# Kernel optimization log

Measured on AMD Instinct MI355X. Metric: run time of the kernel, lower is better.

Reference implementation:

```python
import jax, jax.numpy as jnp
import numpy as np

N = 48
E = N * (N - 1)
H_LSTM = 32
EPS = 20.0

def _conv1d(x, w, b):
    # x: [B, Cin, L], w: [Cout, Cin, K] -> [B, Cout, L], 'same' padding
    y = jax.lax.conv_general_dilated(x, w, window_strides=(1,), padding='SAME',
                                     dimension_numbers=('NCH', 'OIH', 'NCH'))
    return y + b[None, :, None]

def _map(M, x):
    # map_features: linear map along dim 0 (gather for n_to_e one-hot rows,
    # incidence-sum scatter for e_to_n). M: [O, I], x: [I, ...] -> [O, ...]
    return jnp.tensordot(M, x, axes=1)

def _node_cnn(x, adj, layers, final):
    # graph conv stack: neighbor mix (adj along dim 0) + conv1d over node axis + relu
    nl = len(layers)
    for i, (w, b) in enumerate(layers):
        x = _conv1d(_map(adj, x), w, b)
        if not (final and i == nl - 1):
            x = jax.nn.relu(x)
    return x

def _node_lstm(x, mem, adj, w, b):
    # mem = cat([c, h], dim=1); gates from conv over adj-mixed cat([x, h])
    H = mem.shape[1] // 2
    c, h = mem[:, :H], mem[:, H:]
    gates = _conv1d(_map(adj, jnp.concatenate([x, h], axis=1)), w, b)
    i, f, g, o = jnp.split(gates, 4, axis=1)
    c2 = jax.nn.sigmoid(f) * c + jax.nn.sigmoid(i) * jnp.tanh(g)
    h2 = jax.nn.sigmoid(o) * jnp.tanh(c2)
    return jnp.concatenate([c2, h2], axis=1)

def _forward(bi, bij, msgi, msgj, v, nmem0, emem0, neadj, eeadj,
             e_to_n0, e_to_n1, n_to_e0, n_to_e1, decoding, params):
    fm, efm, nlstm, elstm, pp, epp = params
    n = bi.shape[0]
    e = bij.shape[0]
    # map_node_feature_to_edge
    bi_g1 = _map(n_to_e0, bi)   # [E,1,N]
    bi_g2 = _map(n_to_e1, bi)   # [E,1,N]
    # softmax (logsumexp) message computation over bij [E,1,N,N]
    cmsgi = jax.nn.logsumexp((bi_g2[:, :, None, :] + bij) * EPS, axis=3) / EPS  # [E,1,N]
    cmsgj = jax.nn.logsumexp((bi_g1[:, :, :, None] + bij) * EPS, axis=2) / EPS  # [E,1,N]
    ncmsgi = _map(e_to_n0, cmsgi)
    ncmsgj = _map(e_to_n1, cmsgj)
    nnmsgi = _map(e_to_n0, msgi)
    nnmsgj = _map(e_to_n1, msgj)
    # partial_feature (detached in original)
    dec_mat = jax.nn.one_hot(decoding, n, dtype=bi.dtype)        # [N,N]
    xi = _map(n_to_e0, dec_mat)[:, :, None]                      # [E,N,1]
    xj = _map(n_to_e1, dec_mat)[:, None, :]                      # [E,1,N]
    ep = bij.reshape(e, n, n)
    f1 = jax.lax.stop_gradient(_map(e_to_n0, (ep * xi).sum(axis=1)).reshape(n, 1, n))
    f2 = jax.lax.stop_gradient(_map(e_to_n1, (ep * xj).sum(axis=2)).reshape(n, 1, n))
    node_feature = jnp.concatenate([bi, bi + v, nnmsgi, nnmsgj, ncmsgi, ncmsgj, f1, f2], axis=1)  # [N,8,N]
    edge_feature = jnp.concatenate([msgi, msgj, cmsgi, cmsgj, bi_g1, bi_g2], axis=1)              # [E,6,N]
    nfeat = _node_cnn(node_feature, neadj, fm, False)   # [N,32,N]
    efeat = _node_cnn(edge_feature, eeadj, efm, False)  # [E,32,N]
    ntoe1, ntoe2 = _map(n_to_e0, nfeat), _map(n_to_e1, nfeat)
    eton1, eton2 = _map(e_to_n0, efeat), _map(e_to_n1, efeat)
    nfeat = jnp.concatenate([nfeat, eton1, eton2], axis=1)  # [N,96,N]
    efeat = jnp.concatenate([efeat, ntoe1, ntoe2], axis=1)  # [E,96,N]
    nmem_new = _node_lstm(nfeat, nmem0, neadj, nlstm[0], nlstm[1])  # [N,64,N]
    emem_new = _node_lstm(efeat, emem0, eeadj, elstm[0], elstm[1])  # [E,64,N]
    nfeat = nmem_new[:, H_LSTM:]   # h part
    efeat = emem_new[:, H_LSTM:]
    ntoe1, ntoe2 = _map(n_to_e0, nfeat), _map(n_to_e1, nfeat)
    eton1, eton2 = _map(e_to_n0, efeat), _map(e_to_n1, efeat)
    nfeat = jnp.concatenate([nfeat, eton1, eton2], axis=1)
    efeat = jnp.concatenate([efeat, ntoe1, ntoe2], axis=1)
    efeat = _node_cnn(efeat, eeadj, epp, True)   # [E,2,N]
    nfeat = _node_cnn(nfeat, neadj, pp, True)    # [N,1,N]
    nmsgi = efeat[:, 0:1] + 0.5 * cmsgi - msgi
    nmsgj = efeat[:, 1:2] + 0.5 * cmsgj - msgj
    nv = nfeat.mean(axis=0, keepdims=True)       # [1,1,N]
    v_out = v + nv
    bij_out = bij - nmsgi.reshape(e, 1, n, 1) - nmsgj.reshape(e, 1, 1, n)
    bi_out = bi + _map(e_to_n0, nmsgi) + _map(e_to_n1, nmsgj) - nv
    msgi_out = msgi + nmsgi
    msgj_out = msgj + nmsgj
    # get_current_dual (softmax=True)
    cdual = (v_out.sum()
             + jax.nn.logsumexp(bi_out.reshape(-1, n) * EPS, axis=1).sum() / EPS
             + jax.nn.logsumexp(bij_out.reshape(-1, n * n) * EPS, axis=1).sum() / EPS)
    return bi_out, bij_out, msgi_out, msgj_out, v_out, cdual, nmem_new, emem_new, f1, f2

def setup_inputs() -> dict:
    key = jax.random.key(0)
    ks = jax.random.split(key, 16)
    ii, jj = np.meshgrid(np.arange(N), np.arange(N), indexing='ij')
    mask = ii != jj
    src, dst = ii[mask], jj[mask]  # [E] complete directed graph
    eye = np.eye(N, dtype=np.float32)
    n_to_e0 = jnp.asarray(eye[src])  # [E,N] one-hot gather
    n_to_e1 = jnp.asarray(eye[dst])
    e_to_n0 = n_to_e0.T              # [N,E] incidence scatter-sum
    e_to_n1 = n_to_e1.T
    def glorot(k, shape):
        fan_in = shape[1] * shape[2]
        return jax.random.normal(k, shape, jnp.float32) / np.sqrt(fan_in)
    pk = jax.random.split(ks[15], 20)
    return dict(
        bi=jax.random.normal(ks[0], (N, 1, N), jnp.float32),
        bij=jax.random.normal(ks[1], (E, 1, N, N), jnp.float32),
        msgi=jnp.zeros((E, 1, N), jnp.float32),
        msgj=jnp.zeros((E, 1, N), jnp.float32),
        v=jnp.zeros((1, 1, N), jnp.float32),
        nmem0=jnp.zeros((N, 2 * H_LSTM, N), jnp.float32),
        emem0=jnp.zeros((E, 2 * H_LSTM, N), jnp.float32),
        neadj=jax.random.uniform(ks[2], (N, N), jnp.float32) / N,
        eeadj=jax.random.uniform(ks[3], (E, E), jnp.float32) / E,
        e_to_n0=e_to_n0, e_to_n1=e_to_n1, n_to_e0=n_to_e0, n_to_e1=n_to_e1,
        decoding=jax.random.randint(ks[4], (N,), 0, N),
        fm_w0=glorot(pk[0], (32, 8, 3)), fm_b0=jnp.zeros((32,), jnp.float32),
        fm_w1=glorot(pk[1], (32, 32, 3)), fm_b1=jnp.zeros((32,), jnp.float32),
        efm_w0=glorot(pk[2], (32, 6, 3)), efm_b0=jnp.zeros((32,), jnp.float32),
        efm_w1=glorot(pk[3], (32, 32, 3)), efm_b1=jnp.zeros((32,), jnp.float32),
        nlstm_w=glorot(pk[4], (128, 128, 3)), nlstm_b=jnp.zeros((128,), jnp.float32),
        elstm_w=glorot(pk[5], (128, 128, 3)), elstm_b=jnp.zeros((128,), jnp.float32),
        pp_w0=glorot(pk[6], (16, 96, 3)), pp_b0=jnp.zeros((16,), jnp.float32),
        pp_w1=glorot(pk[7], (1, 16, 3)), pp_b1=jnp.zeros((1,), jnp.float32),
        epp_w0=glorot(pk[8], (16, 96, 3)), epp_b0=jnp.zeros((16,), jnp.float32),
        epp_w1=glorot(pk[9], (2, 16, 3)), epp_b1=jnp.zeros((2,), jnp.float32),
    )

def reference(bi, bij, msgi, msgj, v, nmem0, emem0, neadj, eeadj,
              e_to_n0, e_to_n1, n_to_e0, n_to_e1, decoding,
              fm_w0, fm_b0, fm_w1, fm_b1, efm_w0, efm_b0, efm_w1, efm_b1,
              nlstm_w, nlstm_b, elstm_w, elstm_b,
              pp_w0, pp_b0, pp_w1, pp_b1, epp_w0, epp_b0, epp_w1, epp_b1):
    params = ([(fm_w0, fm_b0), (fm_w1, fm_b1)],
              [(efm_w0, efm_b0), (efm_w1, efm_b1)],
              (nlstm_w, nlstm_b), (elstm_w, elstm_b),
              [(pp_w0, pp_b0), (pp_w1, pp_b1)],
              [(epp_w0, epp_b0), (epp_w1, epp_b1)])
    return _forward(bi, bij, msgi, msgj, v, nmem0, emem0, neadj, eeadj,
                    e_to_n0, e_to_n1, n_to_e0, n_to_e1, decoding, params)
```

## Files before the change

### kernel.cpp

```cpp
#include <hip/hip_runtime.h>
#include <cstdint>
#include <cstddef>

#define EE 2256
#define EP 2304

typedef __attribute__((ext_vector_type(8))) short bf16x8;
typedef __attribute__((ext_vector_type(4))) float f32x4;

__device__ __forceinline__ unsigned short f2b(float f){
  unsigned u = __builtin_bit_cast(unsigned, f);
  u += 0x7fffu + ((u>>16)&1u);
  return (unsigned short)(u>>16);
}
__device__ __forceinline__ float b2f(unsigned short h){
  unsigned u = ((unsigned)h)<<16; return __builtin_bit_cast(float, u);
}
__device__ __forceinline__ float sigm(float x){ return 1.f/(1.f+__expf(-x)); }
__device__ __forceinline__ float tanhfast(float x){ return 1.f - 2.f/(__expf(2.f*x)+1.f); }

__device__ __forceinline__ int xcd_swz(int bid, int nwg){
  int xcd = bid & 7, idx = bid >> 3;
  int q = nwg >> 3, r = nwg & 7;
  return (xcd < r ? xcd*(q+1) : r*(q+1) + (xcd-r)*q) + idx;
}

typedef __attribute__((address_space(3))) unsigned int lds_u32;
typedef __attribute__((address_space(1))) const unsigned int gbl_u32;
__device__ __forceinline__ void glds16(const void* g, void* l){
  __builtin_amdgcn_global_load_lds((gbl_u32*)g, (lds_u32*)l, 16, 0, 0);
}

__global__ __launch_bounds__(128) void gm_zero_pads(unsigned short* yp6, unsigned short* yp32,
                                                    unsigned short* yp16){
  int e = blockIdx.x; int tid = threadIdx.x;
  #pragma unroll
  for (int r=0; r<2; ++r){
    int row = r ? 49 : 0;
    if (tid < 8)  yp6 [((size_t)e*50+row)*8  + tid] = 0;
    if (tid < 32) yp32[((size_t)e*50+row)*32 + tid] = 0;
    if (tid < 16) yp16[((size_t)e*50+row)*16 + tid] = 0;
  }
}

__global__ __launch_bounds__(128) void gm_zero_pad128(unsigned short* yp128){
  int e = blockIdx.x; int tid = threadIdx.x;
  yp128[((size_t)e*50+0)*128 + tid] = 0;
  yp128[((size_t)e*50+49)*128 + tid] = 0;
}

__global__ void gm_prep_eeadj(const float* __restrict__ src, unsigned short* __restrict__ dst){
  int idx = blockIdx.x*256 + threadIdx.x;
  if (idx >= EP*EP) return;
  int r = idx / EP, k = idx - r*EP;
  float v = (r < EE && k < EE) ? src[(size_t)r*EE + k] : 0.f;
  dst[idx] = f2b(v);
}

__global__ void gm_prep_wall(const float* __restrict__ w0, const float* __restrict__ w1,
                             const float* __restrict__ w2, const float* __restrict__ w3,
                             const float* __restrict__ w4,
                             unsigned short* d0, unsigned short* d1, unsigned short* d2,
                             unsigned short* d3, unsigned short* d4){
  int idx = blockIdx.x*256 + threadIdx.x;
  const float* w; unsigned short* dp; int Co,Cin,KPT,Kpad,loc;
  if      (idx < 1024) { w=w0; dp=d0; Co=32;  Cin=6;   KPT=8;   Kpad=32;  loc=idx; }
  else if (idx < 4096) { w=w1; dp=d1; Co=32;  Cin=32;  KPT=32;  Kpad=96;  loc=idx-1024; }
  else if (idx < 53248){ w=w2; dp=d2; Co=128; Cin=128; KPT=128; Kpad=384; loc=idx-4096; }
  else if (idx < 57856){ w=w3; dp=d3; Co=16;  Cin=96;  KPT=96;  Kpad=288; loc=idx-53248; }
  else if (idx < 58880){ w=w4; dp=d4; Co=2;   Cin=16;  KPT=16;  Kpad=64;  loc=idx-57856; }
  else return;
  int co = loc / Kpad; int k = loc - co*Kpad;
  int t = k / KPT; int ci = k - t*KPT;
  float v = (co < Co && t < 3 && ci < Cin) ? w[((size_t)co*Cin + ci)*3 + t] : 0.f;
  dp[loc] = f2b(v);
}

__global__ __launch_bounds__(128) void gm_cmsg(const float* __restrict__ bi, const float* __restrict__ bij,
                                               float* __restrict__ cmi, float* __restrict__ cmj){
  int e = blockIdx.x; int tid = threadIdx.x;
  __shared__ float t[48*49]; __shared__ float bs[48], bd[48];
  const float* src = bij + (size_t)e*2304;
  for (int i=tid;i<2304;i+=128){ int r=i/48, c=i-r*48; t[r*49+c]=src[i]; }
  if (tid<48){ int s=e/47, m=e-s*47; int d=m+(m>=s); bs[tid]=bi[s*48+tid]; bd[tid]=bi[d*48+tid]; }
  __syncthreads();
  if (tid < 48){
    float mx=-1e30f;
    for (int n=0;n<48;n++) mx = fmaxf(mx, t[tid*49+n]+bd[n]);
    float sm=0.f;
    for (int n=0;n<48;n++) sm += __expf((t[tid*49+n]+bd[n]-mx)*20.f);
    cmi[e*48+tid] = mx + __logf(sm)*(1.f/20.f);
  } else if (tid>=64 && tid<112){
    int n = tid-64;
    float mx=-1e30f;
    for (int k=0;k<48;k++) mx = fmaxf(mx, t[k*49+n]+bs[k]);
    float sm=0.f;
    for (int k=0;k<48;k++) sm += __expf((t[k*49+n]+bs[k]-mx)*20.f);
    cmj[e*48+n] = mx + __logf(sm)*(1.f/20.f);
  }
}

__global__ __launch_bounds__(256) void gm_node_accum(const float* __restrict__ bij, const float* __restrict__ cmi,
                              const float* __restrict__ cmj, const float* __restrict__ msgi,
                              const float* __restrict__ msgj, const int* __restrict__ dec,
                              float* ncmi, float* ncmj, float* nnmi, float* nnmj,
                              float* o_f1, float* o_f2){
  int i = blockIdx.x; int tid = threadIdx.x;
  __shared__ float red[5][6][48];
  int mg = tid / 48;
  int w  = tid - mg*48;
  if (mg < 5){
    int dc = dec[i];
    float a1=0,a2=0,a3=0,a4=0,s1=0,s2=0;
    for (int m=mg; m<47; m+=5){
      int e1 = i*47+m;
      a1 += cmi[e1*48+w]; a3 += msgi[e1*48+w];
      s1 += bij[(size_t)e1*2304 + dc*48 + w];
      int j = m + (m>=i); int e2 = j*47 + i - (i>j);
      a2 += cmj[e2*48+w]; a4 += msgj[e2*48+w];
      s2 += bij[(size_t)e2*2304 + w*48 + dc];
    }
    red[mg][0][w]=a1; red[mg][1][w]=a2; red[mg][2][w]=a3;
    red[mg][3][w]=a4; red[mg][4][w]=s1; red[mg][5][w]=s2;
  }
  __syncthreads();
  if (tid < 48){
    float a1=0,a2=0,a3=0,a4=0,s1=0,s2=0;
    for (int g=0; g<5; g++){
      a1+=red[g][0][tid]; a2+=red[g][1][tid]; a3+=red[g][2][tid];
      a4+=red[g][3][tid]; s1+=red[g][4][tid]; s2+=red[g][5][tid];
    }
    ncmi[i*48+tid]=a1; ncmj[i*48+tid]=a2; nnmi[i*48+tid]=a3; nnmj[i*48+tid]=a4;
    o_f1[i*48+tid]=s1; o_f2[i*48+tid]=s2;
  }
}

__global__ void gm_build_x6(const float* __restrict__ msgi, const float* __restrict__ msgj,
                            const float* __restrict__ cmi, const float* __restrict__ cmj,
                            const float* __restrict__ bi, unsigned short* __restrict__ x6){
  int idx = blockIdx.x*256 + threadIdx.x;
  if (idx >= 288*EP) return;
  int row = idx / EP, e = idx - row*EP;
  int w = row / 6, c = row - w*6;
  unsigned short val = 0;
  if (e < EE){
    int s = e/47, m = e-s*47, d = m + (m>=s);
    float x;
    switch(c){
      case 0: x = msgi[e*48+w]; break;
      case 1: x = msgj[e*48+w]; break;
      case 2: x = cmi[e*48+w]; break;
      case 3: x = cmj[e*48+w]; break;
      case 4: x = bi[s*48+w]; break;
      default: x = bi[d*48+w]; break;
    }
    val = f2b(x);
  }
  x6[idx] = val;
}

__global__ void gm_fill_x128_hi(const float* __restrict__ emem0, const float* __restrict__ nfeat,
                                unsigned short* __restrict__ x128){
  int idx = blockIdx.x*256 + threadIdx.x;
  if (idx >= 96*EP) return;
  int q = idx/EP; int c = 32 + q; int e = idx - q*EP;
  if (e >= EE){ for (int w=0;w<48;w++) x128[(size_t)(w*128+c)*EP + e] = 0; return; }
  int s=e/47, m=e-s*47, d=m+(m>=s);
  const float* srcrow;
  if (c < 64)      srcrow = nfeat + ((size_t)s*32 + (c-32))*48;
  else if (c < 96) srcrow = nfeat + ((size_t)d*32 + (c-64))*48;
  else             srcrow = emem0 + ((size_t)e*64 + (c-64))*48;
  #pragma unroll
  for (int w4=0; w4<12; w4++){
    float4 xv = *(const float4*)(srcrow + w4*4);
    x128[(size_t)((w4*4+0)*128+c)*EP + e] = f2b(xv.x);
    x128[(size_t)((w4*4+1)*128+c)*EP + e] = f2b(xv.y);
    x128[(size_t)((w4*4+2)*128+c)*EP + e] = f2b(xv.z);
    x128[(size_t)((w4*4+3)*128+c)*EP + e] = f2b(xv.w);
  }
}

__global__ __launch_bounds__(256) void gm_map_gemm(
    const unsigned short* __restrict__ A, const unsigned short* __restrict__ BT,
    unsigned short* __restrict__ ypad, float* __restrict__ outf,
    const float* __restrict__ bias, int nrow, int Nvalid, int Cch, int Cslab,
    int do_relu, int f32_out)
{
  __shared__ __align__(16) unsigned short lA[128*32];
  __shared__ __align__(16) unsigned short lB[128*32];
  const int tid = threadIdx.x;
  const int lane = tid & 63, wid = tid >> 6;
  const int swz = xcd_swz(blockIdx.x, gridDim.x);
  const int m0 = (swz % nrow) * 128;
  const int n0 = (swz / nrow) * 128;
  const int wm = wid >> 1, wn = wid & 1;
  f32x4 acc[4][4];
  #pragma unroll
  for (int i=0;i<4;i++){
    #pragma unroll
    for (int j=0;j<4;j++) acc[i][j] = f32x4{0.f,0.f,0.f,0.f};
  }
  const int srow = (lane>>2), scol = (lane&3);

  for (int ks = 0; ks < EP/32; ++ks) {
    #pragma unroll
    for (int q=0;q<2;q++){
      int chunk = wid*2+q;
      int row = chunk*16 + srow;
      int off = (scol*16) ^ (((row>>1)&3)<<4);
      glds16((const char*)A  + (size_t)(m0+row)*(EP*2) + ks*64 + off, (char*)lA + chunk*1024);
      glds16((const char*)BT + (size_t)(n0+row)*(EP*2) + ks*64 + off, (char*)lB + chunk*1024);
    }
    __syncthreads();
    bf16x8 af[4], bfr[4];
    #pragma unroll
    for (int mi=0;mi<4;mi++){
      int row = wm*64 + mi*16 + (lane&15);
      int off = ((lane>>4)*16) ^ (((row>>1)&3)<<4);
      af[mi] = *(const bf16x8*)((const char*)lA + row*64 + off);
    }
    #pragma unroll
    for (int ni=0;ni<4;ni++){
      int row = wn*64 + ni*16 + (lane&15);
      int off = ((lane>>4)*16) ^ (((row>>1)&3)<<4);
      bfr[ni] = *(const bf16x8*)((const char*)lB + row*64 + off);
    }
    #pragma unroll
    for (int mi=0;mi<4;mi++){
      #pragma unroll
      for (int ni=0;ni<4;ni++)
        acc[mi][ni] = __builtin_amdgcn_mfma_f32_16x16x32_bf16(af[mi], bfr[ni], acc[mi][ni], 0,0,0);
    }
    __syncthreads();
  }
  #pragma unroll
  for (int mi=0;mi<4;mi++){
    int ebase = m0 + wm*64 + mi*16 + (lane>>4)*4;
    #pragma unroll
    for (int ni=0;ni<4;ni++){
      int c = n0 + wn*64 + ni*16 + (lane&15);
      if (c >= Nvalid) continue;
      int w = c / Cch, ci = c - w*Cch;
      float bv = bias ? bias[ci] : 0.f;
      #pragma unroll
      for (int r=0;r<4;r++){
        int e = ebase + r;
        if (e >= EE) continue;
        float x = acc[mi][ni][r] + bv;
        if (do_relu) x = fmaxf(x, 0.f);
        if (f32_out) outf[(size_t)e*Nvalid + c] = x;
        else ypad[((size_t)e*50 + 1 + w)*Cslab + ci] = f2b(x);
      }
    }
  }
}

__global__ __launch_bounds__(256) void gm_map_sk(
    const unsigned short* __restrict__ A, const unsigned short* __restrict__ BT,
    float* __restrict__ pbuf, int nrow, int ncol, int S, int kspan)
{
  __shared__ __align__(16) unsigned short lA[128*32];
  __shared__ __align__(16) unsigned short lB[128*32];
  const int tid = threadIdx.x;
  const int lane = tid & 63, wid = tid >> 6;
  const int swz = xcd_swz(blockIdx.x, gridDim.x);
  const int ntile = nrow*ncol;
  const int sp = swz / ntile;
  const int tile = swz - sp*ntile;
  const int m0 = (tile % nrow) * 128;
  const int n0 = (tile / nrow) * 128;
  const int Npad = ncol*128;
  const int k0 = sp*kspan, k1 = k0 + kspan;
  const int wm = wid >> 1, wn = wid & 1;
  f32x4 acc[4][4];
  #pragma unroll
  for (int i=0;i<4;i++){
    #pragma unroll
    for (int j=0;j<4;j++) acc[i][j] = f32x4{0.f,0.f,0.f,0.f};
  }
  const int srow = (lane>>2), scol = (lane&3);

  for (int ks = k0; ks < k1; ++ks){
    #pragma unroll
    for (int q=0;q<2;q++){
      int chunk = wid*2+q;
      int row = chunk*16 + srow;
      int off = (scol*16) ^ (((row>>1)&3)<<4);
      glds16((const char*)A  + (size_t)(m0+row)*(EP*2) + ks*64 + off, (char*)lA + chunk*1024);
      glds16((const char*)BT + (size_t)(n0+row)*(EP*2) + ks*64 + off, (char*)lB + chunk*1024);
    }
    __syncthreads();
    bf16x8 af[4], bfr[4];
    #pragma unroll
    for (int mi=0;mi<4;mi++){
      int row = wm*64 + mi*16 + (lane&15);
      int off = ((lane>>4)*16) ^ (((row>>1)&3)<<4);
      af[mi] = *(const bf16x8*)((const char*)lA + row*64 + off);
    }
    #pragma unroll
    for (int ni=0;ni<4;ni++){
      int row = wn*64 + ni*16 + (lane&15);
      int off = ((lane>>4)*16) ^ (((row>>1)&3)<<4);
      bfr[ni] = *(const bf16x8*)((const char*)lB + row*64 + off);
    }
    #pragma unroll
    for (int mi=0;mi<4;mi++){
      #pragma unroll
      for (int ni=0;ni<4;ni++)
        acc[mi][ni] = __builtin_amdgcn_mfma_f32_16x16x32_bf16(af[mi], bfr[ni], acc[mi][ni], 0,0,0);
    }
    __syncthreads();
  }
  float* pb = pbuf + (size_t)sp*2304*Npad;
  #pragma unroll
  for (int mi=0;mi<4;mi++){
    int ebase = m0 + wm*64 + mi*16 + (lane>>4)*4;
    #pragma unroll
    for (int ni=0;ni<4;ni++){
      int c = n0 + wn*64 + ni*16 + (lane&15);
      #pragma unroll
      for (int r=0;r<4;r++)
        pb[(size_t)(ebase+r)*Npad + c] = acc[mi][ni][r];
    }
  }
}

__global__ void gm_sk_fin(const float* __restrict__ pbuf, unsigned short* __restrict__ ypad,
                          float* __restrict__ outf, const float* __restrict__ bias,
                          int S, int Npad, int Nvalid, int Cch, int Cslab, int do_relu, int f32_out){
  int idx = blockIdx.x*256 + threadIdx.x;
  if (idx >= EE*Nvalid) return;
  int e = idx / Nvalid, c = idx - e*Nvalid;
  float s = 0.f;
  for (int p=0;p<S;p++) s += pbuf[(size_t)p*2304*Npad + (size_t)e*Npad + c];
  int w = c / Cch, ci = c - w*Cch;
  if (bias) s += bias[ci];
  if (do_relu) s = fmaxf(s, 0.f);
  if (f32_out) outf[(size_t)e*Nvalid + c] = s;
  else ypad[((size_t)e*50 + 1 + w)*Cslab + ci] = f2b(s);
}

template<int BM>
__global__ __launch_bounds__(256) void gm_conv_gemm(
    const unsigned short* __restrict__ Wp, const unsigned short* __restrict__ ypad,
    unsigned short* __restrict__ outT, const float* __restrict__ bias,
    int Cch, int KPT, int Kpad, int Co, int Ct, int do_relu)
{
  constexpr int MI = (BM==128)?4:((BM==32)?2:1);
  constexpr int NI = (BM==128)?4:2;
  __shared__ __align__(16) unsigned short lA[BM*32];
  __shared__ __align__(16) unsigned short lB[128*32];
  const int tid = threadIdx.x, lane = tid&63, wid = tid>>6;
  const int swz = xcd_swz(blockIdx.x, 864);
  const int e0 = (swz / 48) * 128;
  const int w  = swz % 48;
  const int rowb = (BM==128)? (wid>>1)*64 : 0;
  const int colb = (BM==128)? (wid&1)*64 : wid*32;
  f32x4 acc[MI][NI];
  #pragma unroll
  for (int i=0;i<MI;i++){
    #pragma unroll
    for (int j=0;j<NI;j++) acc[i][j] = f32x4{0.f,0.f,0.f,0.f};
  }
  const int srow=(lane>>2), scol=(lane&3);
  const int ksteps = Kpad/32;
  for (int ks=0; ks<ksteps; ++ks){
    for (int c = wid; c < BM/16; c += 4){
      int row = c*16 + srow;
      int off = (scol*16) ^ (((row>>1)&3)<<4);
      glds16((const char*)Wp + (size_t)row*(Kpad*2) + ks*64 + off, (char*)lA + c*1024);
    }
    for (int c = wid; c < 8; c += 4){
      int row = c*16 + srow;
      int off = (scol*16) ^ (((row>>1)&3)<<4);
      int kg = ks*32 + (off>>1);
      int t = kg / KPT;
      int ci = kg - t*KPT;
      int e = e0 + row;
      const char* src;
      if (t < 3 && e < EE) src = (const char*)ypad + ((size_t)(e*50 + w + t)*Cch + ci)*2;
      else                 src = (const char*)ypad;
      glds16(src, (char*)lB + c*1024);
    }
    __syncthreads();
    bf16x8 af[MI], bfr[NI];
    #pragma unroll
    for (int mi=0;mi<MI;mi++){
      int row = rowb + mi*16 + (lane&15);
      int off = ((lane>>4)*16) ^ (((row>>1)&3)<<4);
      af[mi] = *(const bf16x8*)((const char*)lA + row*64 + off);
    }
    #pragma unroll
    for (int ni=0;ni<NI;ni++){
      int row = colb + ni*16 + (lane&15);
      int off = ((lane>>4)*16) ^ (((row>>1)&3)<<4);
      bfr[ni] = *(const bf16x8*)((const char*)lB + row*64 + off);
    }
    #pragma unroll
    for (int mi=0;mi<MI;mi++){
      #pragma unroll
      for (int ni=0;ni<NI;ni++)
        acc[mi][ni] = __builtin_amdgcn_mfma_f32_16x16x32_bf16(af[mi], bfr[ni], acc[mi][ni], 0,0,0);
    }
    __syncthreads();
  }
  #pragma unroll
  for (int mi=0;mi<MI;mi++){
    #pragma unroll
    for (int ni=0;ni<NI;ni++){
      int m = colb + ni*16 + (lane&15);
      int e = e0 + m;
      if (e >= EE) continue;
      #pragma unroll
      for (int r=0;r<4;r++){
        int co = rowb + mi*16 + (lane>>4)*4 + r;
        if (co >= Co) continue;
        float x = acc[mi][ni][r] + (bias ? bias[co] : 0.f);
        if (do_relu) x = fmaxf(x, 0.f);
        outT[((size_t)(w*Ct + co))*EP + e] = f2b(x);
      }
    }
  }
}

__global__ void gm_build_nf(const float* __restrict__ bi, const float* __restrict__ v,
                            const float* __restrict__ nnmi, const float* __restrict__ nnmj,
                            const float* __restrict__ ncmi, const float* __restrict__ ncmj,
                            const float* __restrict__ f1, const float* __restrict__ f2,
                            float* __restrict__ nf){
  int idx = blockIdx.x*256+threadIdx.x;
  if (idx >= 48*8*48) return;
  int i = idx/(8*48); int rem = idx - i*(8*48); int c = rem/48; int w = rem-c*48;
  int iw = i*48+w;
  float x;
  switch(c){
    case 0: x=bi[iw]; break;
    case 1: x=bi[iw]+v[w]; break;
    case 2: x=nnmi[iw]; break;
    case 3: x=nnmj[iw]; break;
    case 4: x=ncmi[iw]; break;
    case 5: x=ncmj[iw]; break;
    case 6: x=f1[iw]; break;
    default: x=f2[iw]; break;
  }
  nf[idx]=x;
}

__global__ void gm_nmap(const float* __restrict__ adj, const float* __restrict__ X,
                        float* __restrict__ Y, int C){
  int idx = blockIdx.x*256 + threadIdx.x;
  int tot = 48*C*48;
  if (idx >= tot) return;
  int i = idx/(C*48); int rem = idx - i*(C*48);
  float s=0.f;
  for (int j=0;j<48;j++) s += adj[i*48+j]*X[(size_t)j*C*48 + rem];
  Y[idx]=s;
}

__global__ void gm_nconv(const float* __restrict__ X, const float* __restrict__ wgt,
                         const float* __restrict__ bias, float* __restrict__ Y,
                         int Cin, int Co, int relu){
  int idx = blockIdx.x*256 + threadIdx.x;
  int tot = 48*Co*48;
  if (idx >= tot) return;
  int i = idx/(Co*48); int rem = idx - i*(Co*48); int co = rem/48; int w = rem-co*48;
  float s = bias[co];
  const float* xb = X + (size_t)i*Cin*48;
  const float* wb = wgt + (size_t)co*Cin*3;
  for (int ci=0; ci<Cin; ++ci){
    float w0 = wb[ci*3], w1 = wb[ci*3+1], w2 = wb[ci*3+2];
    const float* xr = xb + ci*48;
    if (w > 0) s += xr[w-1]*w0;
    s += xr[w]*w1;
    if (w < 47) s += xr[w+1]*w2;
  }
  if (relu) s = fmaxf(s, 0.f);
  Y[idx] = s;
}

__global__ __launch_bounds__(256) void gm_nconv_lstm(const float* __restrict__ X,
    const float* __restrict__ wgt, const float* __restrict__ bias,
    const float* __restrict__ nmem0, float* __restrict__ o_nmem, float* __restrict__ nfeat2){
  int idx = blockIdx.x*256 + threadIdx.x;
  if (idx >= 48*32*48) return;
  int i = idx/(32*48); int rem = idx - i*(32*48); int ch = rem/48; int w = rem-ch*48;
  const float* xb = X + (size_t)i*128*48;
  float s0=bias[ch], s1=bias[32+ch], s2=bias[64+ch], s3=bias[96+ch];
  for (int ci=0; ci<128; ++ci){
    const float* xr = xb + ci*48;
    float xm = (w>0)? xr[w-1] : 0.f;
    float xc = xr[w];
    float xp = (w<47)? xr[w+1] : 0.f;
    const float* wb0 = wgt + ((size_t)ch*128+ci)*3;
    const float* wb1 = wgt + ((size_t)(32+ch)*128+ci)*3;
    const float* wb2 = wgt + ((size_t)(64+ch)*128+ci)*3;
    const float* wb3 = wgt + ((size_t)(96+ch)*128+ci)*3;
    s0 += xm*wb0[0]+xc*wb0[1]+xp*wb0[2];
    s1 += xm*wb1[0]+xc*wb1[1]+xp*wb1[2];
    s2 += xm*wb2[0]+xc*wb2[1]+xp*wb2[2];
    s3 += xm*wb3[0]+xc*wb3[1]+xp*wb3[2];
  }
  float c = nmem0[((size_t)i*64+ch)*48+w];
  float c2 = sigm(s1)*c + sigm(s0)*tanhfast(s2);
  float h2 = sigm(s3)*tanhfast(c2);
  o_nmem[((size_t)i*64+ch)*48+w] = c2;
  o_nmem[((size_t)i*64+32+ch)*48+w] = h2;
  nfeat2[((size_t)i*32+ch)*48+w] = h2;
}

__global__ __launch_bounds__(256) void gm_eton_x128(const unsigned short* __restrict__ x128,
                                                    float* __restrict__ xn){
  int row = blockIdx.x;
  int w = row >> 5, cc = row & 31;
  __shared__ float L[2256];
  const unsigned short* src = x128 + (size_t)(w*128 + cc)*EP;
  for (int t=threadIdx.x; t<2256; t+=256) L[t] = b2f(src[t]);
  __syncthreads();
  int tid = threadIdx.x;
  if (tid < 48){
    int i = tid; float s=0.f;
    for (int m=0;m<47;m++) s += L[i*47+m];
    xn[((size_t)i*128 + 32 + cc)*48 + w] = s;
  } else if (tid >= 64 && tid < 112){
    int i = tid-64; float s=0.f;
    for (int m=0;m<47;m++){
      int j = m + (m>=i);
      s += L[j*47 + i - (i>j)];
    }
    xn[((size_t)i*128 + 64 + cc)*48 + w] = s;
  }
}

__global__ void gm_xnode_copy(const float* __restrict__ nfeat, const float* __restrict__ nmem0,
                              float* __restrict__ xn){
  int idx = blockIdx.x*256+threadIdx.x;
  if (idx >= 48*64*48) return;
  int i = idx/(64*48); int rem = idx - i*(64*48); int c = rem/48; int w = rem-c*48;
  if (c < 32) xn[((size_t)i*128 + c)*48 + w] = nfeat[((size_t)i*32+c)*48+w];
  else        xn[((size_t)i*128 + 96 + (c-32))*48 + w] = nmem0[((size_t)i*64 + 32 + (c-32))*48 + w];
}

__global__ __launch_bounds__(256) void gm_elstm_pw(const unsigned short* __restrict__ gatesT,
                                                   const float* __restrict__ emem0,
                                                   float* __restrict__ o_emem){
  int bid = blockIdx.x;
  int e4 = bid / 6, chunk = bid - e4*6;
  int cw = chunk*256 + threadIdx.x;
  int ch = cw / 48, w = cw - ch*48;
  int ebase = e4*4;
  const unsigned short* g0 = gatesT + (size_t)(w*128 + ch)*EP + ebase;
  ushort4 vi = *(const ushort4*)(g0);
  ushort4 vf = *(const ushort4*)(g0 + (size_t)32*EP);
  ushort4 vg = *(const ushort4*)(g0 + (size_t)64*EP);
  ushort4 vo = *(const ushort4*)(g0 + (size_t)96*EP);
  const unsigned short* pi = (const unsigned short*)&vi;
  const unsigned short* pf = (const unsigned short*)&vf;
  const unsigned short* pg = (const unsigned short*)&vg;
  const unsigned short* po = (const unsigned short*)&vo;
  #pragma unroll
  for (int r=0;r<4;r++){
    int e = ebase + r;
    float gi = b2f(pi[r]), gf = b2f(pf[r]), gg = b2f(pg[r]), go = b2f(po[r]);
    float c  = emem0[((size_t)e*64 + ch)*48 + w];
    float c2 = sigm(gf)*c + sigm(gi)*tanhfast(gg);
    float h2 = sigm(go)*tanhfast(c2);
    o_emem[((size_t)e*64 + ch)*48 + w] = c2;
    o_emem[((size_t)e*64 + 32+ch)*48 + w] = h2;
  }
}

__global__ __launch_bounds__(256) void gm_eton_h(const float* __restrict__ o_emem,
                                                 float* __restrict__ x2){
  int row = blockIdx.x; int w = row >> 5, cc = row & 31;
  __shared__ float L[2256];
  for (int t=threadIdx.x; t<2256; t+=256)
    L[t] = o_emem[((size_t)t*64 + 32 + cc)*48 + w];
  __syncthreads();
  int tid = threadIdx.x;
  if (tid < 48){
    int i=tid; float s=0.f;
    for (int m=0;m<47;m++) s += L[i*47+m];
    x2[((size_t)i*96 + 32 + cc)*48 + w] = s;
  } else if (tid>=64 && tid<112){
    int i=tid-64; float s=0.f;
    for (int m=0;m<47;m++){ int j=m+(m>=i); s += L[j*47 + i - (i>j)]; }
    x2[((size_t)i*96 + 64 + cc)*48 + w] = s;
  }
}

__global__ void gm_x2_copy(const float* __restrict__ nfeat2, float* __restrict__ x2){
  int idx = blockIdx.x*256+threadIdx.x;
  if (idx >= 48*32*48) return;
  int i = idx/(32*48); int rem = idx - i*(32*48); int c = rem/48; int w = rem-c*48;
  x2[((size_t)i*96 + c)*48 + w] = nfeat2[idx];
}

__global__ __launch_bounds__(128) void gm_build_xpp(const float* __restrict__ o_emem,
                                                    const float* __restrict__ nfeat2,
                                                    unsigned short* __restrict__ xpp){
  int e = blockIdx.x; int tid = threadIdx.x;
  __shared__ float h[1536];
  __shared__ float sn[3072];
  int s = e/47; int m = e - s*47; int d = m + (m>=s);
  const float* src = o_emem + ((size_t)e*64 + 32)*48;
  for (int i=tid;i<1536;i+=128) h[i]=src[i];
  const float* ps = nfeat2 + (size_t)s*32*48;
  const float* pd = nfeat2 + (size_t)d*32*48;
  for (int i=tid;i<1536;i+=128){ sn[i]=ps[i]; sn[1536+i]=pd[i]; }
  if (tid < 96){
    xpp[((size_t)e*50 + 0)*96 + tid] = 0;
    xpp[((size_t)e*50 + 49)*96 + tid] = 0;
  }
  __syncthreads();
  for (int w=0; w<48; w++){
    if (tid < 96){
      float x;
      if (tid<32) x = h[tid*48+w];
      else x = sn[(tid-32)*48 + w];
      xpp[((size_t)e*50 + 1 + w)*96 + tid] = f2b(x);
    }
  }
}

__global__ void gm_nv(const float* __restrict__ nfpp, const float* __restrict__ v,
                      float* __restrict__ nv, float* __restrict__ o_v){
  int w = threadIdx.x;
  if (w<48){
    float s=0.f; for (int i=0;i<48;i++) s += nfpp[i*48+w];
    s *= (1.f/48.f);
    nv[w]=s; o_v[w]=v[w]+s;
  }
}

__global__ __launch_bounds__(256) void gm_bijout(const float* __restrict__ bij,
                                                 const float* __restrict__ effpp,
                                                 const float* __restrict__ cmi, const float* __restrict__ cmj,
                                                 const float* __restrict__ msgi, const float* __restrict__ msgj,
                                                 float* __restrict__ nmi, float* __restrict__ nmj,
                                                 float* __restrict__ o_mi, float* __restrict__ o_mj,
                                                 float* __restrict__ o_bij, float* __restrict__ lse_e){
  int e = blockIdx.x; int tid = threadIdx.x;
  __shared__ float ri[48], rj[48], red[8];
  if (tid < 48){
    int idx = e*48+tid;
    float a = effpp[(size_t)e*96 + tid*2] + 0.5f*cmi[idx] - msgi[idx];
    ri[tid] = a; nmi[idx] = a; o_mi[idx] = msgi[idx] + a;
  } else if (tid >= 64 && tid < 112){
    int t2 = tid-64; int idx = e*48+t2;
    float b = effpp[(size_t)e*96 + t2*2 + 1] + 0.5f*cmj[idx] - msgj[idx];
    rj[t2] = b; nmj[idx] = b; o_mj[idx] = msgj[idx] + b;
  }
  __syncthreads();
  float v[9]; float mx = -1e30f;
  const float* src = bij + (size_t)e*2304;
  float* dst = o_bij + (size_t)e*2304;
  #pragma unroll
  for (int q=0;q<9;q++){
    int idx = q*256 + tid;
    int r = idx/48, c = idx-r*48;
    float x = src[idx] - ri[r] - rj[c];
    dst[idx] = x; v[q] = x; mx = fmaxf(mx, x);
  }
  for (int o=1;o<64;o<<=1) mx = fmaxf(mx, __shfl_xor(mx, o, 64));
  int lane = tid&63, w4 = tid>>6;
  if (lane==0) red[w4] = mx;
  __syncthreads();
  mx = fmaxf(fmaxf(red[0],red[1]),fmaxf(red[2],red[3]));
  float s = 0.f;
  #pragma unroll
  for (int q=0;q<9;q++) s += __expf((v[q]-mx)*20.f);
  for (int o=1;o<64;o<<=1) s += __shfl_xor(s, o, 64);
  if (lane==0) red[4+w4] = s;
  __syncthreads();
  if (tid==0){
    float t = red[4]+red[5]+red[6]+red[7];
    lse_e[e] = mx + __logf(t)*(1.f/20.f);
  }
}

__global__ void gm_biout(const float* __restrict__ bi, const float* __restrict__ nmi,
                         const float* __restrict__ nmj, const float* __restrict__ nv,
                         float* __restrict__ o_bi, float* __restrict__ lse_n){
  int i = blockIdx.x; int w = threadIdx.x;
  float val = -1e30f;
  if (w < 48){
    float s = 0.f;
    for (int m=0;m<47;m++){
      int e1 = i*47+m;
      s += nmi[e1*48+w];
      int j = m + (m>=i);
      int e2 = j*47 + i - (i>j);
      s += nmj[e2*48+w];
    }
    val = bi[i*48+w] + s - nv[w];
    o_bi[i*48+w] = val;
  }
  float mx = val;
  for (int o=1;o<64;o<<=1) mx = fmaxf(mx, __shfl_xor(mx, o, 64));
  float ex = (w<48)? __expf((val-mx)*20.f) : 0.f;
  for (int o=1;o<64;o<<=1) ex += __shfl_xor(ex, o, 64);
  if (w==0) lse_n[i] = mx + __logf(ex)*(1.f/20.f);
}

__global__ void gm_cdual(const float* __restrict__ lse_e, const float* __restrict__ lse_n,
                         const float* __restrict__ vout, float* __restrict__ out){
  int tid = threadIdx.x;
  float s = 0.f;
  for (int i=tid;i<EE;i+=256) s += lse_e[i];
  if (tid<48) s += lse_n[tid] + vout[tid];
  __shared__ float red[4];
  for (int o=1;o<64;o<<=1) s += __shfl_xor(s,o,64);
  if ((tid&63)==0) red[tid>>6]=s;
  __syncthreads();
  if (tid==0) out[0] = red[0]+red[1]+red[2]+red[3];
}

static constexpr size_t A256v(size_t x){ return (x+255)&~(size_t)255; }
static constexpr size_t OFF_EEADJ = 0;
static constexpr size_t OFF_X6T   = A256v(OFF_EEADJ + (size_t)EP*EP*2);
static constexpr size_t OFF_X32T  = A256v(OFF_X6T  + (size_t)384*EP*2);
static constexpr size_t OFF_X128T = A256v(OFF_X32T + (size_t)1536*EP*2);
static constexpr size_t OFF_YP6   = A256v(OFF_X128T + (size_t)6144*EP*2);
static constexpr size_t OFF_YP32  = A256v(OFF_YP6  + (size_t)EE*50*8*2);
static constexpr size_t OFF_YP128 = A256v(OFF_YP32 + (size_t)EE*50*32*2);
static constexpr size_t OFF_YP16  = A256v(OFF_YP128 + (size_t)EE*50*128*2);
static constexpr size_t OFF_ZEND  = A256v(OFF_YP16 + (size_t)EE*50*16*2 + 256);
static constexpr size_t OFF_XPP   = OFF_YP128;
static constexpr size_t OFF_SKP   = OFF_YP128;
static constexpr size_t OFF_WC0 = OFF_ZEND;
static constexpr size_t OFF_WC1 = A256v(OFF_WC0 + 32*32*2);
static constexpr size_t OFF_WCL = A256v(OFF_WC1 + 32*96*2);
static constexpr size_t OFF_WP0 = A256v(OFF_WCL + 128*384*2);
static constexpr size_t OFF_WP1 = A256v(OFF_WP0 + 16*288*2);
static constexpr size_t OFF_CMI = A256v(OFF_WP1 + 16*64*2);
static constexpr size_t OFF_CMJ = A256v(OFF_CMI + (size_t)EE*48*4);
static constexpr size_t OFF_NMI = A256v(OFF_CMJ + (size_t)EE*48*4);
static constexpr size_t OFF_NMJ = A256v(OFF_NMI + (size_t)EE*48*4);
static constexpr size_t OFF_EFPP= A256v(OFF_NMJ + (size_t)EE*48*4);
static constexpr size_t OFF_LSEE= A256v(OFF_EFPP + (size_t)EE*96*4);
static constexpr size_t OFF_LSEN= A256v(OFF_LSEE + EE*4);
static constexpr size_t OFF_NV  = A256v(OFF_LSEN + 48*4);
static constexpr size_t OFF_NF  = A256v(OFF_NV + 48*4);
static constexpr size_t OFF_NT1 = A256v(OFF_NF + (size_t)48*8*48*4);
static constexpr size_t OFF_NT2 = A256v(OFF_NT1 + (size_t)48*128*48*4);
static constexpr size_t OFF_NFEAT = A256v(OFF_NT2 + (size_t)48*32*48*4);
static constexpr size_t OFF_NFEAT2= A256v(OFF_NFEAT + (size_t)48*32*48*4);
static constexpr size_t OFF_XN  = A256v(OFF_NFEAT2 + (size_t)48*32*48*4);
static constexpr size_t OFF_NFPP= A256v(OFF_XN + (size_t)48*128*48*4);
static constexpr size_t OFF_NAC = A256v(OFF_NFPP + (size_t)48*48*4);

extern "C" void kernel_launch(void* const* d_in, const int* in_sizes, int n_in,
                              void* d_out, int out_size, void* d_ws, size_t ws_size,
                              hipStream_t stream) {
  const float* bi    = (const float*)d_in[0];
  const float* bij   = (const float*)d_in[1];
  const float* msgi  = (const float*)d_in[2];
  const float* msgj  = (const float*)d_in[3];
  const float* v_in  = (const float*)d_in[4];
  const float* nmem0 = (const float*)d_in[5];
  const float* emem0 = (const float*)d_in[6];
  const float* neadj = (const float*)d_in[7];
  const float* eeadj = (const float*)d_in[8];
  const int*   dec   = (const int*)d_in[13];
  const float* fm_w0 = (const float*)d_in[14]; const float* fm_b0 = (const float*)d_in[15];
  const float* fm_w1 = (const float*)d_in[16]; const float* fm_b1 = (const float*)d_in[17];
  const float* efm_w0= (const float*)d_in[18]; const float* efm_b0= (const float*)d_in[19];
  const float* efm_w1= (const float*)d_in[20]; const float* efm_b1= (const float*)d_in[21];
  const float* nl_w  = (const float*)d_in[22]; const float* nl_b  = (const float*)d_in[23];
  const float* el_w  = (const float*)d_in[24]; const float* el_b  = (const float*)d_in[25];
  const float* pp_w0 = (const float*)d_in[26]; const float* pp_b0 = (const float*)d_in[27];
  const float* pp_w1 = (const float*)d_in[28]; const float* pp_b1 = (const float*)d_in[29];
  const float* epp_w0= (const float*)d_in[30]; const float* epp_b0= (const float*)d_in[31];
  const float* epp_w1= (const float*)d_in[32]; const float* epp_b1= (const float*)d_in[33];

  char* ws = (char*)d_ws;
  unsigned short* eeadjb = (unsigned short*)(ws + OFF_EEADJ);
  unsigned short* x6t    = (unsigned short*)(ws + OFF_X6T);
  unsigned short* x32t   = (unsigned short*)(ws + OFF_X32T);
  unsigned short* x128t  = (unsigned short*)(ws + OFF_X128T);
  unsigned short* z1t    = x32t;
  unsigned short* z2t    = x6t;
  unsigned short* gatesT = x128t;
  unsigned short* yp6    = (unsigned short*)(ws + OFF_YP6);
  unsigned short* yp32   = (unsigned short*)(ws + OFF_YP32);
  unsigned short* yp128  = (unsigned short*)(ws + OFF_YP128);
  unsigned short* yp16   = (unsigned short*)(ws + OFF_YP16);
  unsigned short* xpp    = (unsigned short*)(ws + OFF_XPP);
  float*          skp    = (float*)(ws + OFF_SKP);
  unsigned short* wc0 = (unsigned short*)(ws + OFF_WC0);
  unsigned short* wc1 = (unsigned short*)(ws + OFF_WC1);
  unsigned short* wcl = (unsigned short*)(ws + OFF_WCL);
  unsigned short* wp0 = (unsigned short*)(ws + OFF_WP0);
  unsigned short* wp1 = (unsigned short*)(ws + OFF_WP1);
  float* cmi  = (float*)(ws + OFF_CMI);
  float* cmj  = (float*)(ws + OFF_CMJ);
  float* nmi  = (float*)(ws + OFF_NMI);
  float* nmj  = (float*)(ws + OFF_NMJ);
  float* effpp= (float*)(ws + OFF_EFPP);
  float* lse_e= (float*)(ws + OFF_LSEE);
  float* lse_n= (float*)(ws + OFF_LSEN);
  float* nvb  = (float*)(ws + OFF_NV);
  float* nf   = (float*)(ws + OFF_NF);
  float* nt1  = (float*)(ws + OFF_NT1);
  float* nt2  = (float*)(ws + OFF_NT2);
  float* nfeat  = (float*)(ws + OFF_NFEAT);
  float* nfeat2 = (float*)(ws + OFF_NFEAT2);
  float* xn   = (float*)(ws + OFF_XN);
  float* nfpp = (float*)(ws + OFF_NFPP);
  float* ncmi = (float*)(ws + OFF_NAC);
  float* ncmj = ncmi + 2304;
  float* nnmi = ncmi + 2*2304;
  float* nnmj = ncmi + 3*2304;

  float* out = (float*)d_out;
  float* o_bi   = out;
  float* o_bij  = out + 2304;
  float* o_mi   = out + 2304 + 5197824;
  float* o_mj   = o_mi + 108288;
  float* o_v    = o_mj + 108288;
  float* o_cd   = o_v + 48;
  float* o_nmem = o_cd + 1;
  float* o_emem = o_nmem + 147456;
  float* o_f1   = o_emem + 6930432;
  float* o_f2   = o_f1 + 2304;

  gm_zero_pads<<<EE, 128, 0, stream>>>(yp6, yp32, yp16);
  gm_prep_eeadj<<<(EP*EP+255)/256, 256, 0, stream>>>(eeadj, eeadjb);
  gm_prep_wall<<<(58880+255)/256, 256, 0, stream>>>(efm_w0, efm_w1, el_w, epp_w0, epp_w1,
                                                    wc0, wc1, wcl, wp0, wp1);
  gm_cmsg<<<EE, 128, 0, stream>>>(bi, bij, cmi, cmj);
  gm_node_accum<<<48, 256, 0, stream>>>(bij, cmi, cmj, msgi, msgj, dec, ncmi, ncmj, nnmi, nnmj, o_f1, o_f2);
  gm_build_x6<<<(288*EP+255)/256, 256, 0, stream>>>(msgi, msgj, cmi, cmj, bi, x6t);
  gm_build_nf<<<(48*8*48+255)/256, 256, 0, stream>>>(bi, v_in, nnmi, nnmj, ncmi, ncmj, o_f1, o_f2, nf);
  gm_nmap<<<(48*8*48+255)/256, 256, 0, stream>>>(neadj, nf, nt1, 8);
  gm_nconv<<<(48*32*48+255)/256, 256, 0, stream>>>(nt1, fm_w0, fm_b0, nt2, 8, 32, 1);
  gm_nmap<<<(48*32*48+255)/256, 256, 0, stream>>>(neadj, nt2, nt1, 32);
  gm_nconv<<<(48*32*48+255)/256, 256, 0, stream>>>(nt1, fm_w1, fm_b1, nfeat, 32, 32, 1);
  gm_map_sk<<<216, 256, 0, stream>>>(eeadjb, x6t, skp, 18, 3, 4, 18);
  gm_sk_fin<<<(EE*288+255)/256, 256, 0, stream>>>(skp, yp6, nullptr, nullptr, 4, 384, 288, 6, 8, 0, 0);
  gm_conv_gemm<32><<<864, 256, 0, stream>>>(wc0, yp6,  x32t, efm_b0, 8, 8, 32, 32, 32, 1);
  gm_map_gemm<<<216, 256, 0, stream>>>(eeadjb, x32t, yp32, nullptr, nullptr, 18, 1536, 32, 32, 0, 0);
  gm_conv_gemm<32><<<864, 256, 0, stream>>>(wc1, yp32, x128t, efm_b1, 32, 32, 96, 32, 128, 1);
  gm_fill_x128_hi<<<(96*EP+255)/256, 256, 0, stream>>>(emem0, nfeat, x128t);
  gm_xnode_copy<<<(48*64*48+255)/256, 256, 0, stream>>>(nfeat, nmem0, xn);
  gm_eton_x128<<<1536, 256, 0, stream>>>(x128t, xn);
  gm_nmap<<<(48*128*48+255)/256, 256, 0, stream>>>(neadj, xn, nt1, 128);
  gm_nconv_lstm<<<(48*32*48+255)/256, 256, 0, stream>>>(nt1, nl_w, nl_b, nmem0, o_nmem, nfeat2);
  gm_zero_pad128<<<EE, 128, 0, stream>>>(yp128);
  gm_map_gemm<<<864, 256, 0, stream>>>(eeadjb, x128t, yp128, nullptr, nullptr, 18, 6144, 128, 128, 0, 0);
  gm_conv_gemm<128><<<864, 256, 0, stream>>>(wcl, yp128, gatesT, el_b, 128, 128, 384, 128, 128, 0);
  gm_elstm_pw<<<564*6, 256, 0, stream>>>(gatesT, emem0, o_emem);
  gm_build_xpp<<<EE, 128, 0, stream>>>(o_emem, nfeat2, xpp);
  gm_conv_gemm<16><<<864, 256, 0, stream>>>(wp0, xpp,  z1t, nullptr, 96, 96, 288, 16, 16, 0);
  gm_map_sk<<<432, 256, 0, stream>>>(eeadjb, z1t, skp, 18, 6, 4, 18);
  gm_sk_fin<<<(EE*768+255)/256, 256, 0, stream>>>(skp, yp16, nullptr, epp_b0, 4, 768, 768, 16, 16, 1, 0);
  gm_conv_gemm<16><<<864, 256, 0, stream>>>(wp1, yp16, z2t, nullptr, 16, 16, 64, 2, 2, 0);
  gm_map_sk<<<144, 256, 0, stream>>>(eeadjb, z2t, skp, 18, 1, 8, 9);
  gm_sk_fin<<<(EE*96+255)/256, 256, 0, stream>>>(skp, nullptr, effpp, epp_b1, 8, 128, 96, 2, 2, 0, 1);
  gm_x2_copy<<<(48*32*48+255)/256, 256, 0, stream>>>(nfeat2, xn);
  gm_eton_h<<<1536, 256, 0, stream>>>(o_emem, xn);
  gm_nmap<<<(48*96*48+255)/256, 256, 0, stream>>>(neadj, xn, nt1, 96);
  gm_nconv<<<(48*16*48+255)/256, 256, 0, stream>>>(nt1, pp_w0, pp_b0, nt2, 96, 16, 1);
  gm_nmap<<<(48*16*48+255)/256, 256, 0, stream>>>(neadj, nt2, nt1, 16);
  gm_nconv<<<(48*1*48+255)/256, 256, 0, stream>>>(nt1, pp_w1, pp_b1, nfpp, 16, 1, 0);
  gm_nv<<<1, 64, 0, stream>>>(nfpp, v_in, nvb, o_v);
  gm_bijout<<<EE, 256, 0, stream>>>(bij, effpp, cmi, cmj, msgi, msgj, nmi, nmj, o_mi, o_mj, o_bij, lse_e);
  gm_biout<<<48, 64, 0, stream>>>(bi, nmi, nmj, nvb, o_bi, lse_n);
  gm_cdual<<<1, 256, 0, stream>>>(lse_e, lse_n, o_v, o_cd);
}
```

Before: 795.4 us.

## Double GEMM K-tile to 64 with XOR swizzle and fuse h into xpp

The two edge-adjacency GEMM kernels now stage a 64-wide K slice per iteration instead of 32, using a new XOR swizzle for shared-memory layout. This halves the number of barrier pairs per tile and does two MFMA sub-steps per load. Split-K spans are halved to match, and the last split-K launch is re-partitioned into 12 splits. The LSTM pointwise kernel also writes h directly into the xpp bf16 buffer, so the build_xpp kernel no longer re-reads h from global memory. Shared memory per block doubles, which may reduce occupancy.

```diff
diff --git a/kernel.cpp b/kernel.cpp
--- a/kernel.cpp
+++ b/kernel.cpp
@@ -186,8 +186,8 @@
     const float* __restrict__ bias, int nrow, int Nvalid, int Cch, int Cslab,
     int do_relu, int f32_out)
 {
-  __shared__ __align__(16) unsigned short lA[128*32];
-  __shared__ __align__(16) unsigned short lB[128*32];
+  __shared__ __align__(16) unsigned short lA[128*64];
+  __shared__ __align__(16) unsigned short lB[128*64];
   const int tid = threadIdx.x;
   const int lane = tid & 63, wid = tid >> 6;
   const int swz = xcd_swz(blockIdx.x, gridDim.x);
@@ -200,36 +200,37 @@
     #pragma unroll
     for (int j=0;j<4;j++) acc[i][j] = f32x4{0.f,0.f,0.f,0.f};
   }
-  const int srow = (lane>>2), scol = (lane&3);
-
-  for (int ks = 0; ks < EP/32; ++ks) {
-    #pragma unroll
-    for (int q=0;q<2;q++){
-      int chunk = wid*2+q;
-      int row = chunk*16 + srow;
-      int off = (scol*16) ^ (((row>>1)&3)<<4);
-      glds16((const char*)A  + (size_t)(m0+row)*(EP*2) + ks*64 + off, (char*)lA + chunk*1024);
-      glds16((const char*)BT + (size_t)(n0+row)*(EP*2) + ks*64 + off, (char*)lB + chunk*1024);
+  const int srcc = (((lane&7) ^ (lane>>3))<<4);
+
+  for (int ks = 0; ks < EP/64; ++ks) {
+    #pragma unroll
+    for (int c = wid; c < 16; c += 4){
+      int row = c*8 + (lane>>3);
+      glds16((const char*)A  + (size_t)(m0+row)*(EP*2) + ks*128 + srcc, (char*)lA + c*1024);
+      glds16((const char*)BT + (size_t)(n0+row)*(EP*2) + ks*128 + srcc, (char*)lB + c*1024);
     }
     __syncthreads();
-    bf16x8 af[4], bfr[4];
-    #pragma unroll
-    for (int mi=0;mi<4;mi++){
-      int row = wm*64 + mi*16 + (lane&15);
-      int off = ((lane>>4)*16) ^ (((row>>1)&3)<<4);
-      af[mi] = *(const bf16x8*)((const char*)lA + row*64 + off);
-    }
-    #pragma unroll
-    for (int ni=0;ni<4;ni++){
-      int row = wn*64 + ni*16 + (lane&15);
-      int off = ((lane>>4)*16) ^ (((row>>1)&3)<<4);
-      bfr[ni] = *(const bf16x8*)((const char*)lB + row*64 + off);
-    }
-    #pragma unroll
-    for (int mi=0;mi<4;mi++){
-      #pragma unroll
-      for (int ni=0;ni<4;ni++)
-        acc[mi][ni] = __builtin_amdgcn_mfma_f32_16x16x32_bf16(af[mi], bfr[ni], acc[mi][ni], 0,0,0);
+    #pragma unroll
+    for (int kk=0; kk<2; ++kk){
+      bf16x8 af[4], bfr[4];
+      #pragma unroll
+      for (int mi=0;mi<4;mi++){
+        int row = wm*64 + mi*16 + (lane&15);
+        int sc = ((lane>>4)*16 + kk*64) ^ ((row&7)<<4);
+        af[mi] = *(const bf16x8*)((const char*)lA + row*128 + sc);
+      }
+      #pragma unroll
+      for (int ni=0;ni<4;ni++){
+        int row = wn*64 + ni*16 + (lane&15);
+        int sc = ((lane>>4)*16 + kk*64) ^ ((row&7)<<4);
+        bfr[ni] = *(const bf16x8*)((const char*)lB + row*128 + sc);
+      }
+      #pragma unroll
+      for (int mi=0;mi<4;mi++){
+        #pragma unroll
+        for (int ni=0;ni<4;ni++)
+          acc[mi][ni] = __builtin_amdgcn_mfma_f32_16x16x32_bf16(af[mi], bfr[ni], acc[mi][ni], 0,0,0);
+      }
     }
     __syncthreads();
   }
@@ -259,8 +260,8 @@
     const unsigned short* __restrict__ A, const unsigned short* __restrict__ BT,
     float* __restrict__ pbuf, int nrow, int ncol, int S, int kspan)
 {
-  __shared__ __align__(16) unsigned short lA[128*32];
-  __shared__ __align__(16) unsigned short lB[128*32];
+  __shared__ __align__(16) unsigned short lA[128*64];
+  __shared__ __align__(16) unsigned short lB[128*64];
   const int tid = threadIdx.x;
   const int lane = tid & 63, wid = tid >> 6;
   const int swz = xcd_swz(blockIdx.x, gridDim.x);
@@ -278,36 +279,37 @@
     #pragma unroll
     for (int j=0;j<4;j++) acc[i][j] = f32x4{0.f,0.f,0.f,0.f};
   }
-  const int srow = (lane>>2), scol = (lane&3);
+  const int srcc = (((lane&7) ^ (lane>>3))<<4);
 
   for (int ks = k0; ks < k1; ++ks){
     #pragma unroll
-    for (int q=0;q<2;q++){
-      int chunk = wid*2+q;
-      int row = chunk*16 + srow;
-      int off = (scol*16) ^ (((row>>1)&3)<<4);
-      glds16((const char*)A  + (size_t)(m0+row)*(EP*2) + ks*64 + off, (char*)lA + chunk*1024);
-      glds16((const char*)BT + (size_t)(n0+row)*(EP*2) + ks*64 + off, (char*)lB + chunk*1024);
+    for (int c = wid; c < 16; c += 4){
+      int row = c*8 + (lane>>3);
+      glds16((const char*)A  + (size_t)(m0+row)*(EP*2) + ks*128 + srcc, (char*)lA + c*1024);
+      glds16((const char*)BT + (size_t)(n0+row)*(EP*2) + ks*128 + srcc, (char*)lB + c*1024);
     }
     __syncthreads();
-    bf16x8 af[4], bfr[4];
-    #pragma unroll
-    for (int mi=0;mi<4;mi++){
-      int row = wm*64 + mi*16 + (lane&15);
-      int off = ((lane>>4)*16) ^ (((row>>1)&3)<<4);
-      af[mi] = *(const bf16x8*)((const char*)lA + row*64 + off);
-    }
-    #pragma unroll
-    for (int ni=0;ni<4;ni++){
-      int row = wn*64 + ni*16 + (lane&15);
-      int off = ((lane>>4)*16) ^ (((row>>1)&3)<<4);
-      bfr[ni] = *(const bf16x8*)((const char*)lB + row*64 + off);
-    }
-    #pragma unroll
-    for (int mi=0;mi<4;mi++){
-      #pragma unroll
-      for (int ni=0;ni<4;ni++)
-        acc[mi][ni] = __builtin_amdgcn_mfma_f32_16x16x32_bf16(af[mi], bfr[ni], acc[mi][ni], 0,0,0);
+    #pragma unroll
+    for (int kk=0; kk<2; ++kk){
+      bf16x8 af[4], bfr[4];
+      #pragma unroll
+      for (int mi=0;mi<4;mi++){
+        int row = wm*64 + mi*16 + (lane&15);
+        int sc = ((lane>>4)*16 + kk*64) ^ ((row&7)<<4);
+        af[mi] = *(const bf16x8*)((const char*)lA + row*128 + sc);
+      }
+      #pragma unroll
+      for (int ni=0;ni<4;ni++){
+        int row = wn*64 + ni*16 + (lane&15);
+        int sc = ((lane>>4)*16 + kk*64) ^ ((row&7)<<4);
+        bfr[ni] = *(const bf16x8*)((const char*)lB + row*128 + sc);
+      }
+      #pragma unroll
+      for (int mi=0;mi<4;mi++){
+        #pragma unroll
+        for (int ni=0;ni<4;ni++)
+          acc[mi][ni] = __builtin_amdgcn_mfma_f32_16x16x32_bf16(af[mi], bfr[ni], acc[mi][ni], 0,0,0);
+      }
     }
     __syncthreads();
   }
@@ -542,7 +544,8 @@
 
 __global__ __launch_bounds__(256) void gm_elstm_pw(const unsigned short* __restrict__ gatesT,
                                                    const float* __restrict__ emem0,
-                                                   float* __restrict__ o_emem){
+                                                   float* __restrict__ o_emem,
+                                                   unsigned short* __restrict__ xpp){
   int bid = blockIdx.x;
   int e4 = bid / 6, chunk = bid - e4*6;
   int cw = chunk*256 + threadIdx.x;
@@ -566,6 +569,7 @@
     float h2 = sigm(go)*tanhfast(c2);
     o_emem[((size_t)e*64 + ch)*48 + w] = c2;
     o_emem[((size_t)e*64 + 32+ch)*48 + w] = h2;
+    xpp[((size_t)e*50 + 1 + w)*96 + ch] = f2b(h2);
   }
 }
 
@@ -595,15 +599,11 @@
   x2[((size_t)i*96 + c)*48 + w] = nfeat2[idx];
 }
 
-__global__ __launch_bounds__(128) void gm_build_xpp(const float* __restrict__ o_emem,
-                                                    const float* __restrict__ nfeat2,
-                                                    unsigned short* __restrict__ xpp){
+__global__ __launch_bounds__(128) void gm_build_xpp2(const float* __restrict__ nfeat2,
+                                                     unsigned short* __restrict__ xpp){
   int e = blockIdx.x; int tid = threadIdx.x;
-  __shared__ float h[1536];
   __shared__ float sn[3072];
   int s = e/47; int m = e - s*47; int d = m + (m>=s);
-  const float* src = o_emem + ((size_t)e*64 + 32)*48;
-  for (int i=tid;i<1536;i+=128) h[i]=src[i];
   const float* ps = nfeat2 + (size_t)s*32*48;
   const float* pd = nfeat2 + (size_t)d*32*48;
   for (int i=tid;i<1536;i+=128){ sn[i]=ps[i]; sn[1536+i]=pd[i]; }
@@ -613,11 +613,8 @@
   }
   __syncthreads();
   for (int w=0; w<48; w++){
-    if (tid < 96){
-      float x;
-      if (tid<32) x = h[tid*48+w];
-      else x = sn[(tid-32)*48 + w];
-      xpp[((size_t)e*50 + 1 + w)*96 + tid] = f2b(x);
+    if (tid < 64){
+      xpp[((size_t)e*50 + 1 + w)*96 + 32 + tid] = f2b(sn[tid*48 + w]);
     }
   }
 }
@@ -836,7 +833,7 @@
   gm_nconv<<<(48*32*48+255)/256, 256, 0, stream>>>(nt1, fm_w0, fm_b0, nt2, 8, 32, 1);
   gm_nmap<<<(48*32*48+255)/256, 256, 0, stream>>>(neadj, nt2, nt1, 32);
   gm_nconv<<<(48*32*48+255)/256, 256, 0, stream>>>(nt1, fm_w1, fm_b1, nfeat, 32, 32, 1);
-  gm_map_sk<<<216, 256, 0, stream>>>(eeadjb, x6t, skp, 18, 3, 4, 18);
+  gm_map_sk<<<216, 256, 0, stream>>>(eeadjb, x6t, skp, 18, 3, 4, 9);
   gm_sk_fin<<<(EE*288+255)/256, 256, 0, stream>>>(skp, yp6, nullptr, nullptr, 4, 384, 288, 6, 8, 0, 0);
   gm_conv_gemm<32><<<864, 256, 0, stream>>>(wc0, yp6,  x32t, efm_b0, 8, 8, 32, 32, 32, 1);
   gm_map_gemm<<<216, 256, 0, stream>>>(eeadjb, x32t, yp32, nullptr, nullptr, 18, 1536, 32, 32, 0, 0);
@@ -849,14 +846,14 @@
   gm_zero_pad128<<<EE, 128, 0, stream>>>(yp128);
   gm_map_gemm<<<864, 256, 0, stream>>>(eeadjb, x128t, yp128, nullptr, nullptr, 18, 6144, 128, 128, 0, 0);
   gm_conv_gemm<128><<<864, 256, 0, stream>>>(wcl, yp128, gatesT, el_b, 128, 128, 384, 128, 128, 0);
-  gm_elstm_pw<<<564*6, 256, 0, stream>>>(gatesT, emem0, o_emem);
-  gm_build_xpp<<<EE, 128, 0, stream>>>(o_emem, nfeat2, xpp);
+  gm_elstm_pw<<<564*6, 256, 0, stream>>>(gatesT, emem0, o_emem, xpp);
+  gm_build_xpp2<<<EE, 128, 0, stream>>>(nfeat2, xpp);
   gm_conv_gemm<16><<<864, 256, 0, stream>>>(wp0, xpp,  z1t, nullptr, 96, 96, 288, 16, 16, 0);
-  gm_map_sk<<<432, 256, 0, stream>>>(eeadjb, z1t, skp, 18, 6, 4, 18);
+  gm_map_sk<<<432, 256, 0, stream>>>(eeadjb, z1t, skp, 18, 6, 4, 9);
   gm_sk_fin<<<(EE*768+255)/256, 256, 0, stream>>>(skp, yp16, nullptr, epp_b0, 4, 768, 768, 16, 16, 1, 0);
   gm_conv_gemm<16><<<864, 256, 0, stream>>>(wp1, yp16, z2t, nullptr, 16, 16, 64, 2, 2, 0);
-  gm_map_sk<<<144, 256, 0, stream>>>(eeadjb, z2t, skp, 18, 1, 8, 9);
-  gm_sk_fin<<<(EE*96+255)/256, 256, 0, stream>>>(skp, nullptr, effpp, epp_b1, 8, 128, 96, 2, 2, 0, 1);
+  gm_map_sk<<<216, 256, 0, stream>>>(eeadjb, z2t, skp, 18, 1, 12, 3);
+  gm_sk_fin<<<(EE*96+255)/256, 256, 0, stream>>>(skp, nullptr, effpp, epp_b1, 12, 128, 96, 2, 2, 0, 1);
   gm_x2_copy<<<(48*32*48+255)/256, 256, 0, stream>>>(nfeat2, xn);
   gm_eton_h<<<1536, 256, 0, stream>>>(o_emem, xn);
   gm_nmap<<<(48*96*48+255)/256, 256, 0, stream>>>(neadj, xn, nt1, 96);
```

New measurement: 789.8 us. No clear change (-0.7%).
